# Performance work log

Hardware: AMD Instinct MI355X
Metric: run time of the kernel (lower is better)

## Reference

```python
import jax, jax.numpy as jnp
import numpy as np

D = (96, 96, 96)          # per-item tensor shape (input_shape)
BATCH = 8
R1, R2 = 32, 16           # ranks for the two multi-resolution partitions
MAX_ITER = 15             # fixed ALS iteration count (torch default 100 w/ early stop)


def setup_inputs() -> dict:
    key = jax.random.key(0)
    k = jax.random.split(key, 5)
    m, n = D[0], D[1] * D[2]  # unfold: (first mode, rest) -> (96, 9216)
    return {
        "x": jax.random.normal(k[0], (BATCH,) + D, dtype=jnp.float32),
        "A0_1": jax.random.normal(k[1], (m, R1), dtype=jnp.float32),
        "B0_1": jax.random.normal(k[2], (n, R1), dtype=jnp.float32),
        "A0_2": jax.random.normal(k[3], (m, R2), dtype=jnp.float32),
        "B0_2": jax.random.normal(k[4], (n, R2), dtype=jnp.float32),
    }


def _clean(f):
    # torch.nan_to_num(f, nan=0.0, posinf=1e10, neginf=-1e10)
    return jnp.nan_to_num(f, nan=0.0, posinf=1e10, neginf=-1e10)


def _als(X, A, B):
    """2-mode PARAFAC == ALS matrix factorization. X: (m,n), A: (m,r), B: (n,r)."""
    def step(carry, _):
        A, B = carry
        # mode 0: khatri-rao prod is just B; V = B^T B; A = (X B) pinv(V)
        A = _clean((X @ B) @ jnp.linalg.pinv(B.T @ B))
        # mode 1: unfold is X^T; V = A^T A; B = (X^T A) pinv(V)
        B = _clean((X.T @ A) @ jnp.linalg.pinv(A.T @ A))
        return (A, B), None
    (A, B), _ = jax.lax.scan(step, (A, B), None, length=MAX_ITER)
    return A, B


def _per_item(t, A0_1, B0_1, A0_2, B0_2):
    m = D[0]
    # partition 1 ([[0],[1,2]]): unfold -> (96, 9216)
    X1 = t.reshape(m, -1)
    A1, B1 = _als(X1, A0_1, B0_1)
    approx1 = (A1 @ B1.T).reshape(D)
    residual = t - approx1
    # partition 2 ([[0,1],[2]]): same identity mode order -> same unfold shape
    X2 = residual.reshape(m, -1)
    A2, B2 = _als(X2, A0_2, B0_2)
    approx2 = (A2 @ B2.T).reshape(D)
    # reconstruct() = sum of partition approximations
    return approx1 + approx2


def reference(x, A0_1, B0_1, A0_2, B0_2):
    # per-item MRLR reconstruction, vmapped over the batch (torch loops per item)
    return jax.vmap(_per_item, in_axes=(0, None, None, None, None))(
        x, A0_1, B0_1, A0_2, B0_2
    )
```

## Files before the change

kernel.cpp:

```cpp
#include <hip/hip_runtime.h>


#define TID ((int)threadIdx.x)
typedef float4 f4;

#define SC27 (1.0f/134217728.0f)

__device__ __forceinline__ f4 ld4(const float* p) { return *(const f4*)p; }
__device__ __forceinline__ void st4(float* p, f4 v) { *(f4*)p = v; }
__device__ __forceinline__ f4 f4zero() { return make_float4(0.f,0.f,0.f,0.f); }
__device__ __forceinline__ f4 add4(f4 a, f4 b){ return make_float4(a.x+b.x,a.y+b.y,a.z+b.z,a.w+b.w); }
__device__ __forceinline__ f4 sub4(f4 a, f4 b){ return make_float4(a.x-b.x,a.y-b.y,a.z-b.z,a.w-b.w); }
__device__ __forceinline__ f4 scl4(f4 a, float s){ return make_float4(a.x*s,a.y*s,a.z*s,a.w*s); }
__device__ __forceinline__ void fma4(f4& a, float s, f4 v) {
  a.x = fmaf(s,v.x,a.x); a.y = fmaf(s,v.y,a.y); a.z = fmaf(s,v.z,a.z); a.w = fmaf(s,v.w,a.w);
}
__device__ __forceinline__ float dot4(f4 a, f4 b, float acc) {
  acc = fmaf(a.x,b.x,acc); acc = fmaf(a.y,b.y,acc);
  acc = fmaf(a.z,b.z,acc); acc = fmaf(a.w,b.w,acc); return acc;
}
__device__ __forceinline__ void trimap(int t, int& ti, int& tj) {
  int rem = t; ti = 0;
  #pragma unroll
  for (int r = 0; r < 12; ++r) { int w = 12 - r; if (rem < w) { ti = r; break; } rem -= w; }
  tj = ti + rem;
}
__device__ __forceinline__ void init8(f4 acc[8][2]) {
  #pragma unroll
  for (int a = 0; a < 8; ++a) { acc[a][0] = f4zero(); acc[a][1] = f4zero(); }
}
__device__ __forceinline__ void tile8_step(f4 acc[8][2], const float* u, const float* v) {
  f4 u0 = ld4(u), u1 = ld4(u+4), v0 = ld4(v), v1 = ld4(v+4);
  float aa[8] = {u0.x,u0.y,u0.z,u0.w,u1.x,u1.y,u1.z,u1.w};
  #pragma unroll
  for (int a = 0; a < 8; ++a) { fma4(acc[a][0], aa[a], v0); fma4(acc[a][1], aa[a], v1); }
}

__global__ __launch_bounds__(512) void k1_partials(
    const float* __restrict__ x, const float* __restrict__ b01,
    const float* __restrict__ b02, float* __restrict__ part,
    int nch, int nsc) {
  __shared__ __align__(16) float Xst[48][100];
  __shared__ __align__(16) float Bs[48][52];
  __shared__ __align__(16) float red[9600];
  int bid = blockIdx.x;
  int item = bid & 7, kc = bid >> 3;
  const float* X = x + (size_t)item * 96 * 9216;
  float* base = part + (size_t)(item * nch + kc) * 9600;

  int t = TID, kh = 0, tt = 0;
  const float* ap = nullptr; const float* bp = nullptr;
  float* op = nullptr; int os = 0; bool isM = false;
  bool active = (t < 450);
  if (active) {
    kh = t / 150; tt = t % 150;
    if (tt < 78) {
      int ti, tj; trimap(tt, ti, tj);
      ap = &Xst[0][ti*8]; bp = &Xst[0][tj*8];
      op = base + tt*64; os = 8; isM = true;
    } else {
      int u = tt - 78; int i0 = (u/6)*8, c0 = (u%6)*8;
      ap = &Xst[0][i0]; bp = &Bs[0][c0];
      op = base + 4992 + i0*48 + c0; os = 48;
    }
  }

  f4 acc[8][2]; init8(acc);

  for (int sc = 0; sc < nsc; ++sc) {
    int k0 = (kc * nsc + sc) * 48;
    __syncthreads();
    for (int e = TID; e < 1152; e += 512) {
      int i = e / 12, kq = (e % 12) * 4;
      f4 v = ld4(&X[(size_t)i * 9216 + k0 + kq]);
      Xst[kq][i] = v.x; Xst[kq+1][i] = v.y; Xst[kq+2][i] = v.z; Xst[kq+3][i] = v.w;
    }
    for (int e = TID; e < 384; e += 512) {
      int kk = e / 8, cq = (e % 8) * 4;
      st4(&Bs[kk][cq], ld4(&b01[(size_t)(k0 + kk) * 32 + cq]));
    }
    for (int e = TID; e < 192; e += 512) {
      int kk = e / 4, cq = (e % 4) * 4;
      st4(&Bs[kk][32+cq], ld4(&b02[(size_t)(k0 + kk) * 16 + cq]));
    }
    __syncthreads();
    if (active) {
      int asr = 100, bsr = isM ? 100 : 52;
      const float* ar = ap + kh * asr;
      const float* br = bp + kh * bsr;
      #pragma unroll 4
      for (int kk = kh; kk < 48; kk += 3) {
        tile8_step(acc, ar, br);
        ar += 3 * asr; br += 3 * bsr;
      }
    }
  }
  __syncthreads();
  if (active && kh == 1) {
    #pragma unroll
    for (int a = 0; a < 8; ++a) { st4(&red[tt*64+a*8], acc[a][0]); st4(&red[tt*64+a*8+4], acc[a][1]); }
  }
  __syncthreads();
  if (active && kh == 0) {
    #pragma unroll
    for (int a = 0; a < 8; ++a) {
      acc[a][0] = add4(acc[a][0], ld4(&red[tt*64+a*8]));
      acc[a][1] = add4(acc[a][1], ld4(&red[tt*64+a*8+4]));
    }
  }
  __syncthreads();
  if (active && kh == 2) {
    #pragma unroll
    for (int a = 0; a < 8; ++a) { st4(&red[tt*64+a*8], acc[a][0]); st4(&red[tt*64+a*8+4], acc[a][1]); }
  }
  __syncthreads();
  if (active && kh == 0) {
    #pragma unroll
    for (int a = 0; a < 8; ++a) {
      f4 s0 = add4(acc[a][0], ld4(&red[tt*64+a*8]));
      f4 s1 = add4(acc[a][1], ld4(&red[tt*64+a*8+4]));
      st4(op + a*os, s0); st4(op + a*os + 4, s1);
    }
  }
}

__global__ __launch_bounds__(128) void k2_reduce(
    const float* __restrict__ part, float* __restrict__ Mb,
    float* __restrict__ Cb, int nch) {
  int bid = blockIdx.x;
  int item = bid & 7, chunk = bid >> 3;
  if (TID >= 120) return;
  int q4 = chunk * 120 + TID;
  int off = q4 * 4;
  const float* p = part + (size_t)item * nch * 9600 + off;
  f4 s = f4zero();
  #pragma unroll 8
  for (int c = 0; c < nch; ++c) s = add4(s, ld4(p + (size_t)c * 9600));
  if (off < 4992) {
    int tile = off >> 6, w = (off & 63) >> 2;
    int r = w >> 1, cq = (w & 1) * 4;
    int ti, tj; trimap(tile, ti, tj);
    int i = ti*8 + r, j = tj*8 + cq;
    float* Mi = Mb + (size_t)item * 9216;
    st4(&Mi[i*96 + j], s);
    Mi[(j+0)*96 + i] = s.x; Mi[(j+1)*96 + i] = s.y;
    Mi[(j+2)*96 + i] = s.z; Mi[(j+3)*96 + i] = s.w;
  } else {
    st4(&Cb[(size_t)item * 4608 + (off - 4992)], s);
  }
}

__global__ __launch_bounds__(256) void kw_phase(
    const float* __restrict__ Ag, const float* __restrict__ Bg,
    const float* __restrict__ Subg, float* __restrict__ Dg, float scale,
    const float* __restrict__ Tin, int ti_istr, int tis, int tsub,
    float* __restrict__ Tout, int to_istr, int tos, int TW) {
  __shared__ __align__(16) float Bs[96][100];
  __shared__ __align__(16) float As[8][100];
  __shared__ __align__(16) float Ts[96][36];
  int bid = blockIdx.x;
  int item = bid & 7, w = bid >> 3, t = TID;
  const float* A = Ag + (size_t)item * 9216;

  if (w < 12) {
    const float* B = Bg + (size_t)item * 9216;
    for (int e = t; e < 2304; e += 256) {
      int r = e / 24, cq = (e % 24) * 4;
      st4(&Bs[r][cq], ld4(&B[r*96 + cq]));
    }
    if (t < 192) {
      int r = t / 24, cq = (t % 24) * 4;
      st4(&As[r][cq], ld4(&A[(size_t)(w*8 + r)*96 + cq]));
    }
    __syncthreads();
    if (t < 192) {
      int rl = t / 24, jb = (t % 24) * 4;
      f4 acc = f4zero();
      #pragma unroll 8
      for (int k = 0; k < 96; ++k) fma4(acc, As[rl][k], ld4(&Bs[k][jb]));
      int r = w*8 + rl;
      if (Subg) acc = sub4(ld4(&Subg[(size_t)item*9216 + r*96 + jb]), acc);
      else      acc = scl4(acc, scale);
      st4(&Dg[(size_t)item*9216 + r*96 + jb], acc);
    }
  } else {
    for (int e = t; e < 2304; e += 256) {
      int r = e / 24, cq = (e % 24) * 4;
      st4(&Bs[r][cq], ld4(&A[r*96 + cq]));
    }
    int nq = TW >> 2;
    const float* Ti = Tin + (size_t)item * ti_istr;
    for (int e = t; e < 96*nq; e += 256) {
      int r = e / nq, cq = (e % nq) * 4;
      st4(&Ts[r][cq], ld4(&Ti[(size_t)r * tis + cq]));
    }
    __syncthreads();
    int nact = (TW == 32) ? 192 : 96;
    if (t < nact) {
      int r  = (TW == 32) ? (t >> 1) : t;
      int c0 = (TW == 32) ? (t & 1) * 16 : 0;
      f4 acc[4] = {f4zero(), f4zero(), f4zero(), f4zero()};
      #pragma unroll 4
      for (int k = 0; k < 96; ++k) {
        float a = Bs[r][k];
        const float* tr = &Ts[k][c0];
        fma4(acc[0], a, ld4(tr));   fma4(acc[1], a, ld4(tr+4));
        fma4(acc[2], a, ld4(tr+8)); fma4(acc[3], a, ld4(tr+12));
      }
      if (tsub) {
        #pragma unroll
        for (int u = 0; u < 4; ++u) acc[u] = sub4(ld4(&Ts[r][c0 + u*4]), acc[u]);
      }
      float* To = Tout + (size_t)item * to_istr;
      #pragma unroll
      for (int u = 0; u < 4; ++u) st4(&To[(size_t)r * tos + c0 + u*4], acc[u]);
    }
  }
}

template<int R>
__device__ void gj_wave(float* aug, int lane) {
  float col[R];
  if (lane < R) {
    #pragma unroll
    for (int i = 0; i < R; ++i) col[i] = aug[i*68 + lane];
  } else {
    #pragma unroll
    for (int i = 0; i < R; ++i) col[i] = (i == lane - R) ? 1.f : 0.f;
  }
  #pragma unroll
  for (int c = 0; c < R; ++c) {
    float pc = __shfl(col[c], c);
    float rp = 1.f / pc;
    bool isc = (lane == c);
    #pragma unroll
    for (int i = 0; i < R; ++i) {
      if (i == c) continue;
      float fi = __shfl(col[i], c) * rp;
      float v = fmaf(-fi, col[c], col[i]);
      col[i] = isc ? 0.f : v;
    }
  }
  #pragma unroll
  for (int i = 0; i < R; ++i) {
    float d = __shfl(col[i], i);
    col[i] = col[i] / d;
  }
  if (lane >= R) {
    #pragma unroll
    for (int i = 0; i < R; ++i) aug[i*68 + lane] = col[i];
  }
}

template<int TW, int MODE>
__global__ __launch_bounds__(256) void kWproj3(
    const float* __restrict__ Sg, const float* __restrict__ Yg,
    float* __restrict__ W1g, float* __restrict__ Tgg) {
  __shared__ __align__(16) float smem[18944];
  float* St  = smem;
  float* Ta  = smem + 9600;
  float* Tb  = smem + 13056;
  float* aug = smem + 16512;
  float* QKs = smem + 18688;

  int bid = blockIdx.x;
  int item = bid & 7, w = bid >> 3, t = TID;
  const float* S = Sg + (size_t)item * 9216;
  const float* Y = Yg + (size_t)item * 3072;
  float* W1 = W1g + (size_t)item * 9216;
  float* Tg = Tgg + (size_t)item * 9216;
  const int nq = TW >> 2;

  for (int e = t; e < 2304; e += 256) {
    int r = e / 24, cq = (e % 24) * 4;
    f4 v = ld4(&S[r*96 + cq]);
    St[(cq+0)*100 + r] = v.x; St[(cq+1)*100 + r] = v.y;
    St[(cq+2)*100 + r] = v.z; St[(cq+3)*100 + r] = v.w;
  }
  for (int e = t; e < 96*nq; e += 256) {
    int r = e / nq, cq = (e % nq) * 4;
    st4(&Ta[r*36 + cq], ld4(&Y[r*32 + cq]));
  }
  __syncthreads();

  #pragma unroll
  for (int pass = 0; pass < 3; ++pass) {
    const float* src = (pass & 1) ? Tb : Ta;
    float* dst       = (pass & 1) ? Ta : Tb;
    int ntask = 24 * nq;
    if (t < ntask) {
      int rb = (t / nq) * 4, c4 = (t % nq) * 4;
      f4 acc[4] = {f4zero(), f4zero(), f4zero(), f4zero()};
      #pragma unroll 4
      for (int k = 0; k < 96; ++k) {
        f4 s = ld4(&St[k*100 + rb]);
        f4 v = ld4(&src[k*36 + c4]);
        fma4(acc[0], s.x, v); fma4(acc[1], s.y, v);
        fma4(acc[2], s.z, v); fma4(acc[3], s.w, v);
      }
      #pragma unroll
      for (int j = 0; j < 4; ++j) st4(&dst[(rb + j)*36 + c4], acc[j]);
    }
    __syncthreads();
  }

  {
    int na = TW >> 2;
    if (t < na*na) {
      int ab = (t / na) * 4, b4 = (t % na) * 4;
      f4 acc[4] = {f4zero(), f4zero(), f4zero(), f4zero()};
      #pragma unroll 4
      for (int k = 0; k < 96; ++k) {
        f4 qa = ld4(&Tb[k*36 + ab]);
        f4 qb = ld4(&Tb[k*36 + b4]);
        fma4(acc[0], qa.x, qb); fma4(acc[1], qa.y, qb);
        fma4(acc[2], qa.z, qb); fma4(acc[3], qa.w, qb);
      }
      #pragma unroll
      for (int j = 0; j < 4; ++j) st4(&aug[(ab + j)*68 + b4], acc[j]);
    }
  }
  __syncthreads();

  if (t < 2*TW) gj_wave<TW>(aug, t);
  __syncthreads();
  for (int e = t; e < TW*TW; e += 256) {
    int m = e / TW, c = e % TW;
    aug[c*68 + m] = aug[m*68 + TW + c];
  }
  __syncthreads();

  for (int e = t; e < 8*TW; e += 256) {
    int rr = e / TW, c = e % TW;
    float acc = 0.f;
    #pragma unroll
    for (int m4 = 0; m4 < TW; m4 += 4)
      acc = dot4(ld4(&Tb[(w*8 + rr)*36 + m4]), ld4(&aug[c*68 + m4]), acc);
    QKs[rr*32 + c] = acc;
  }
  __syncthreads();

  if (t < 192) {
    int rr = t / 24, jb = (t % 24) * 4;
    int r = w*8 + rr;
    f4 acc = f4zero();
    #pragma unroll
    for (int c4 = 0; c4 < TW; c4 += 4) {
      f4 qk = ld4(&QKs[rr*32 + c4]);
      acc.x = dot4(qk, ld4(&Tb[(jb+0)*36 + c4]), acc.x);
      acc.y = dot4(qk, ld4(&Tb[(jb+1)*36 + c4]), acc.y);
      acc.z = dot4(qk, ld4(&Tb[(jb+2)*36 + c4]), acc.z);
      acc.w = dot4(qk, ld4(&Tb[(jb+3)*36 + c4]), acc.w);
    }
    if (MODE == 1) st4(&W1[r*96 + jb], acc);
    else           st4(&Tg[r*96 + jb], add4(acc, ld4(&W1[r*96 + jb])));
  }
}

__global__ __launch_bounds__(256) void k4_out(
    const float* __restrict__ x, const float* __restrict__ Tgg,
    float* __restrict__ out) {
  __shared__ __align__(16) float Tt[96][100];
  int bid = blockIdx.x;
  int item = bid & 7, jb = bid >> 3;
  const float* Tg = Tgg + (size_t)item * 9216;
  for (int e = TID * 4; e < 9216; e += 1024) {
    f4 v = ld4(&Tg[e]);
    int i = e / 96, k = e % 96;
    Tt[k][i] = v.x; Tt[k+1][i] = v.y; Tt[k+2][i] = v.z; Tt[k+3][i] = v.w;
  }
  __syncthreads();

  int jq = (TID % 32) * 4, ig = TID / 32;
  int i0 = ig * 12;
  int col = jb * 128 + jq;
  const float* X = x + (size_t)item * 96 * 9216;
  f4 acc[12];
  #pragma unroll
  for (int a = 0; a < 12; ++a) acc[a] = f4zero();

  for (int k = 0; k < 96; ++k) {
    f4 xv = ld4(&X[(size_t)k * 9216 + col]);
    f4 t0 = ld4(&Tt[k][i0]), t1 = ld4(&Tt[k][i0+4]), t2 = ld4(&Tt[k][i0+8]);
    fma4(acc[0], t0.x, xv); fma4(acc[1], t0.y, xv); fma4(acc[2], t0.z, xv); fma4(acc[3], t0.w, xv);
    fma4(acc[4], t1.x, xv); fma4(acc[5], t1.y, xv); fma4(acc[6], t1.z, xv); fma4(acc[7], t1.w, xv);
    fma4(acc[8], t2.x, xv); fma4(acc[9], t2.y, xv); fma4(acc[10], t2.z, xv); fma4(acc[11], t2.w, xv);
  }
  float* O = out + (size_t)item * 96 * 9216;
  #pragma unroll
  for (int a = 0; a < 12; ++a) st4(&O[(size_t)(i0 + a) * 9216 + col], acc[a]);
}

extern "C" void kernel_launch(void* const* d_in, const int* in_sizes, int n_in,
                              void* d_out, int out_size, void* d_ws, size_t ws_size,
                              hipStream_t stream) {
  (void)in_sizes; (void)n_in; (void)out_size;
  const float* x   = (const float*)d_in[0];
  const float* b01 = (const float*)d_in[2];
  const float* b02 = (const float*)d_in[4];
  float* out = (float*)d_out;
  float* ws  = (float*)d_ws;

  const size_t EXTRA = 73728ull*5 + 36864 + 24576 + 12288;
  int nch = (ws_size >= ((size_t)64*8*9600 + EXTRA) * sizeof(float)) ? 64 : 32;
  int nsc = 9216 / nch / 48;

  float* Mb  = ws + (size_t)nch * 8 * 9600;
  float* Cb  = Mb  + 73728;
  float* Sb  = Cb  + 36864;
  float* S2b = Sb  + 73728;
  float* W1b = S2b + 73728;
  float* Tgb = W1b + 73728;
  float* Yb  = Tgb + 73728;
  float* CPb = Yb  + 24576;

  k1_partials<<<dim3(nch*8), 512, 0, stream>>>(x, b01, b02, ws, nch, nsc);
  k2_reduce<<<dim3(160), 128, 0, stream>>>(ws, Mb, Cb, nch);

  kw_phase<<<dim3(96),256,0,stream>>>(Mb, Mb, nullptr, Sb, SC27,
      nullptr,0,0,0, nullptr,0,0, 0);
  kw_phase<<<dim3(104),256,0,stream>>>(Sb, Sb, nullptr, S2b, 1.f,
      Cb,4608,48,0, Yb,3072,32, 32);
  kWproj3<32,1><<<dim3(96),256,0,stream>>>(S2b, Yb, W1b, Tgb);

  kw_phase<<<dim3(104),256,0,stream>>>(W1b, Mb, Mb, Sb, 1.f,
      Cb+32,4608,48,1, CPb,1536,16, 16);
  kw_phase<<<dim3(96),256,0,stream>>>(Sb, W1b, Sb, Mb, 1.f,
      nullptr,0,0,0, nullptr,0,0, 0);

  kw_phase<<<dim3(96),256,0,stream>>>(Mb, Mb, nullptr, Sb, SC27,
      nullptr,0,0,0, nullptr,0,0, 0);
  kw_phase<<<dim3(104),256,0,stream>>>(Sb, Sb, nullptr, S2b, 1.f,
      CPb,1536,16,0, Yb,3072,32, 16);
  kWproj3<16,2><<<dim3(96),256,0,stream>>>(S2b, Yb, W1b, Tgb);

  k4_out<<<dim3(576), 256, 0, stream>>>(x, Tgb, out);
}
```

Measured before the change: 174.7 us.

## Split projection kernel into per-item chain and parallel W-build kernels

```diff
diff --git a/kernel.cpp b/kernel.cpp
--- a/kernel.cpp
+++ b/kernel.cpp
@@ -252,23 +252,21 @@
   }
 }
 
-template<int TW, int MODE>
-__global__ __launch_bounds__(256) void kWproj3(
+template<int TW>
+__global__ __launch_bounds__(256) void kB_chain(
     const float* __restrict__ Sg, const float* __restrict__ Yg,
-    float* __restrict__ W1g, float* __restrict__ Tgg) {
-  __shared__ __align__(16) float smem[18944];
+    float* __restrict__ Qg, float* __restrict__ QKg) {
+  __shared__ __align__(16) float smem[18688];
   float* St  = smem;
   float* Ta  = smem + 9600;
   float* Tb  = smem + 13056;
   float* aug = smem + 16512;
-  float* QKs = smem + 18688;
-
-  int bid = blockIdx.x;
-  int item = bid & 7, w = bid >> 3, t = TID;
+
+  int item = blockIdx.x, t = TID;
   const float* S = Sg + (size_t)item * 9216;
   const float* Y = Yg + (size_t)item * 3072;
-  float* W1 = W1g + (size_t)item * 9216;
-  float* Tg = Tgg + (size_t)item * 9216;
+  float* Qo  = Qg  + (size_t)item * 3072;
+  float* QKo = QKg + (size_t)item * 3072;
   const int nq = TW >> 2;
 
   for (int e = t; e < 2304; e += 256) {
@@ -330,13 +328,40 @@
   }
   __syncthreads();
 
-  for (int e = t; e < 8*TW; e += 256) {
-    int rr = e / TW, c = e % TW;
-    float acc = 0.f;
-    #pragma unroll
-    for (int m4 = 0; m4 < TW; m4 += 4)
-      acc = dot4(ld4(&Tb[(w*8 + rr)*36 + m4]), ld4(&aug[c*68 + m4]), acc);
-    QKs[rr*32 + c] = acc;
+  for (int e = t; e < 96*nq; e += 256) {
+    int r = e / nq, c4 = (e % nq) * 4;
+    f4 acc = f4zero();
+    #pragma unroll
+    for (int m4 = 0; m4 < TW; m4 += 4) {
+      f4 qv = ld4(&Tb[r*36 + m4]);
+      acc.x = dot4(qv, ld4(&aug[(c4+0)*68 + m4]), acc.x);
+      acc.y = dot4(qv, ld4(&aug[(c4+1)*68 + m4]), acc.y);
+      acc.z = dot4(qv, ld4(&aug[(c4+2)*68 + m4]), acc.z);
+      acc.w = dot4(qv, ld4(&aug[(c4+3)*68 + m4]), acc.w);
+    }
+    st4(&QKo[r*32 + c4], acc);
+    st4(&Qo[r*32 + c4], ld4(&Tb[r*36 + c4]));
+  }
+}
+
+template<int TW, int MODE>
+__global__ __launch_bounds__(256) void kC_wbuild(
+    const float* __restrict__ Qg, const float* __restrict__ QKg,
+    float* __restrict__ W1g, float* __restrict__ Tgg) {
+  __shared__ __align__(16) float Qs[96][36];
+  __shared__ __align__(16) float QKs[96][36];
+  int bid = blockIdx.x;
+  int item = bid & 7, w = bid >> 3, t = TID;
+  const float* Q  = Qg  + (size_t)item * 3072;
+  const float* QK = QKg + (size_t)item * 3072;
+  float* W1 = W1g + (size_t)item * 9216;
+  float* Tg = Tgg + (size_t)item * 9216;
+  const int nq = TW >> 2;
+
+  for (int e = t; e < 96*nq; e += 256) {
+    int r = e / nq, cq = (e % nq) * 4;
+    st4(&Qs[r][cq],  ld4(&Q[r*32 + cq]));
+    st4(&QKs[r][cq], ld4(&QK[r*32 + cq]));
   }
   __syncthreads();
 
@@ -346,11 +371,11 @@
     f4 acc = f4zero();
     #pragma unroll
     for (int c4 = 0; c4 < TW; c4 += 4) {
-      f4 qk = ld4(&QKs[rr*32 + c4]);
-      acc.x = dot4(qk, ld4(&Tb[(jb+0)*36 + c4]), acc.x);
-      acc.y = dot4(qk, ld4(&Tb[(jb+1)*36 + c4]), acc.y);
-      acc.z = dot4(qk, ld4(&Tb[(jb+2)*36 + c4]), acc.z);
-      acc.w = dot4(qk, ld4(&Tb[(jb+3)*36 + c4]), acc.w);
+      f4 qk = ld4(&QKs[r][c4]);
+      acc.x = dot4(qk, ld4(&Qs[jb+0][c4]), acc.x);
+      acc.y = dot4(qk, ld4(&Qs[jb+1][c4]), acc.y);
+      acc.z = dot4(qk, ld4(&Qs[jb+2][c4]), acc.z);
+      acc.w = dot4(qk, ld4(&Qs[jb+3][c4]), acc.w);
     }
     if (MODE == 1) st4(&W1[r*96 + jb], acc);
     else           st4(&Tg[r*96 + jb], add4(acc, ld4(&W1[r*96 + jb])));
@@ -401,7 +426,7 @@
   float* out = (float*)d_out;
   float* ws  = (float*)d_ws;
 
-  const size_t EXTRA = 73728ull*5 + 36864 + 24576 + 12288;
+  const size_t EXTRA = 73728ull*5 + 36864 + 24576*3 + 12288;
   int nch = (ws_size >= ((size_t)64*8*9600 + EXTRA) * sizeof(float)) ? 64 : 32;
   int nsc = 9216 / nch / 48;
 
@@ -412,7 +437,9 @@
   float* W1b = S2b + 73728;
   float* Tgb = W1b + 73728;
   float* Yb  = Tgb + 73728;
-  float* CPb = Yb  + 24576;
+  float* Qb  = Yb  + 24576;
+  float* QKb = Qb  + 24576;
+  float* CPb = QKb + 24576;
 
   k1_partials<<<dim3(nch*8), 512, 0, stream>>>(x, b01, b02, ws, nch, nsc);
   k2_reduce<<<dim3(160), 128, 0, stream>>>(ws, Mb, Cb, nch);
@@ -421,7 +448,8 @@
       nullptr,0,0,0, nullptr,0,0, 0);
   kw_phase<<<dim3(104),256,0,stream>>>(Sb, Sb, nullptr, S2b, 1.f,
       Cb,4608,48,0, Yb,3072,32, 32);
-  kWproj3<32,1><<<dim3(96),256,0,stream>>>(S2b, Yb, W1b, Tgb);
+  kB_chain<32><<<dim3(8),256,0,stream>>>(S2b, Yb, Qb, QKb);
+  kC_wbuild<32,1><<<dim3(96),256,0,stream>>>(Qb, QKb, W1b, Tgb);
 
   kw_phase<<<dim3(104),256,0,stream>>>(W1b, Mb, Mb, Sb, 1.f,
       Cb+32,4608,48,1, CPb,1536,16, 16);
@@ -432,7 +460,8 @@
       nullptr,0,0,0, nullptr,0,0, 0);
   kw_phase<<<dim3(104),256,0,stream>>>(Sb, Sb, nullptr, S2b, 1.f,
       CPb,1536,16,0, Yb,3072,32, 16);
-  kWproj3<16,2><<<dim3(96),256,0,stream>>>(S2b, Yb, W1b, Tgb);
+  kB_chain<16><<<dim3(8),256,0,stream>>>(S2b, Yb, Qb, QKb);
+  kC_wbuild<16,2><<<dim3(96),256,0,stream>>>(Qb, QKb, W1b, Tgb);
 
   k4_out<<<dim3(576), 256, 0, stream>>>(x, Tgb, out);
 }
```

New measurement: 183.1 us. +4.8%, slower.
